# Optimization experiments

Hardware: AMD Instinct MI355X
Metric: run time of the kernel (lower is better)

Reference implementation:

```python
import jax, jax.numpy as jnp
import numpy as np

ALPHA = 0.2  # LeakyReLU negative slope
NEG_INF = -9e15


def setup_inputs() -> dict:
    key = jax.random.key(0)
    k1, k2, k3, k4 = jax.random.split(key, 4)
    N, F_in, F_out = 8192, 128, 64
    x = jax.random.normal(k1, (N, F_in), dtype=jnp.float32)
    adj = jax.random.randint(k2, (N, N), 0, 2, dtype=jnp.int32)
    W = jax.random.normal(k3, (F_in, F_out), dtype=jnp.float32) * 0.1
    a = jax.random.normal(k4, (2 * F_out, 1), dtype=jnp.float32) * 0.1
    return {"x": x, "adj": adj, "W": W, "a": a}


def reference(x, adj, W, a):
    F_out = W.shape[1]
    Wh = x @ W                         # [N, F_out]
    Wh1 = Wh @ a[:F_out, :]            # [N, 1]
    Wh2 = Wh @ a[F_out:, :]            # [N, 1]
    e = Wh1 + Wh2.T                    # [N, N] broadcast scores
    e = jnp.where(e > 0, e, ALPHA * e) # LeakyReLU
    e = jnp.where(adj > 0, e, NEG_INF) # mask non-edges
    attention = jax.nn.softmax(e, axis=1)
    out = attention @ Wh               # [N, F_out]
    return jax.nn.elu(out)             # concat=True -> ELU
```

## Files before the change

kernel.cpp:

```cpp
#include <hip/hip_runtime.h>
#include <hip/hip_bf16.h>

#define NN 8192
#define FIN 128
#define FOUT 64
#define ALPHA 0.2f
#define BM 64
#define CHUNK 128
#define SPLIT 8
#define JSLICE (NN / SPLIT)
#define NCHUNK (JSLICE / CHUNK)
#define PROW (CHUNK + 8)

typedef __attribute__((ext_vector_type(8))) short short8;
typedef __attribute__((ext_vector_type(4))) float floatx4;

static __device__ __forceinline__ ushort f2bf(float f) {
    __hip_bfloat16 h = __float2bfloat16(f);
    return __builtin_bit_cast(ushort, h);
}

__global__ __launch_bounds__(256) void gat_proj(const float* __restrict__ x,
                                                const float* __restrict__ W,
                                                const float* __restrict__ a,
                                                ushort* __restrict__ WhT,
                                                float* __restrict__ Wh1,
                                                float* __restrict__ Wh2) {
    __shared__ float tile[32][FOUT + 1];

    const int t = threadIdx.x;
    const int f = t & 63;
    const int wv = t >> 6;
    const int row0 = blockIdx.x * 32;
    const float af1 = a[f], af2 = a[FOUT + f];

    for (int r8 = 0; r8 < 8; ++r8) {
        const int row = row0 + wv * 8 + r8;
        const float4* __restrict__ x4 = (const float4*)(x + (size_t)row * FIN);
        float acc = 0.f;
        #pragma unroll
        for (int k4 = 0; k4 < FIN / 4; ++k4) {
            float4 xv = x4[k4];
            const int k = k4 * 4;
            acc = fmaf(xv.x, W[(k + 0) * FOUT + f], acc);
            acc = fmaf(xv.y, W[(k + 1) * FOUT + f], acc);
            acc = fmaf(xv.z, W[(k + 2) * FOUT + f], acc);
            acc = fmaf(xv.w, W[(k + 3) * FOUT + f], acc);
        }
        tile[wv * 8 + r8][f] = acc;

        float s1 = acc * af1;
        float s2 = acc * af2;
        #pragma unroll
        for (int off = 32; off; off >>= 1) {
            s1 += __shfl_xor(s1, off, 64);
            s2 += __shfl_xor(s2, off, 64);
        }
        if (f == 0) { Wh1[row] = s1; Wh2[row] = s2; }
    }
    __syncthreads();

    const int r = t & 31;
    const int fh = t >> 5;
    #pragma unroll
    for (int p = 0; p < 8; ++p) {
        const int ff = p * 8 + fh;
        WhT[(size_t)ff * NN + row0 + r] = f2bf(tile[r][ff]);
    }
}

__global__ __launch_bounds__(256) void gat_attn_part(const int* __restrict__ adj,
                                                     const ushort* __restrict__ WhT,
                                                     const float* __restrict__ Wh1,
                                                     const float* __restrict__ Wh2,
                                                     float* __restrict__ pnum,
                                                     float* __restrict__ pden) {
    __shared__ __align__(16) ushort P[2][BM][PROW];

    const int t = threadIdx.x;
    const int lane = t & 63;
    const int wv = t >> 6;
    const int slice = blockIdx.x & (SPLIT - 1);
    const int row0 = (blockIdx.x / SPLIT) * BM;
    const int j0 = slice * JSLICE;
    const int ln = lane & 15;
    const int quad = lane >> 4;
    const int jg = lane & 31;
    const int rh = lane >> 5;
    const int rbase = wv * 16;

    float wh1r[8];
    #pragma unroll
    for (int rr = 0; rr < 8; ++rr)
        wh1r[rr] = Wh1[row0 + rbase + rh * 8 + rr];

    const int* __restrict__ aptr =
        adj + (size_t)(row0 + rbase + rh * 8) * NN + j0 + jg * 4;

    int4 av[8];
    float4 wh2v;
    auto loadChunk = [&](int c) {
        const int jb = c * CHUNK;
        wh2v = *(const float4*)(Wh2 + j0 + jb + jg * 4);
        #pragma unroll
        for (int rr = 0; rr < 8; ++rr)
            av[rr] = *(const int4*)(aptr + (size_t)rr * NN + jb);
    };

    float den[8];
    #pragma unroll
    for (int rr = 0; rr < 8; ++rr) den[rr] = 0.f;

    auto scoresToLds = [&](int b) {
        #pragma unroll
        for (int rr = 0; rr < 8; ++rr) {
            float s0 = wh1r[rr] + wh2v.x, s1 = wh1r[rr] + wh2v.y,
                  s2 = wh1r[rr] + wh2v.z, s3 = wh1r[rr] + wh2v.w;
            s0 = fmaxf(s0, ALPHA * s0); s1 = fmaxf(s1, ALPHA * s1);
            s2 = fmaxf(s2, ALPHA * s2); s3 = fmaxf(s3, ALPHA * s3);
            float p0 = __expf(s0), p1 = __expf(s1),
                  p2 = __expf(s2), p3 = __expf(s3);
            p0 = (av[rr].x > 0) ? p0 : 0.f; p1 = (av[rr].y > 0) ? p1 : 0.f;
            p2 = (av[rr].z > 0) ? p2 : 0.f; p3 = (av[rr].w > 0) ? p3 : 0.f;
            den[rr] += (p0 + p1) + (p2 + p3);
            ushort4 pk = make_ushort4(f2bf(p0), f2bf(p1), f2bf(p2), f2bf(p3));
            *(ushort4*)&P[b][rbase + rh * 8 + rr][jg * 4] = pk;
        }
    };

    floatx4 acc[4];
    #pragma unroll
    for (int mt = 0; mt < 4; ++mt) acc[mt] = (floatx4){0.f, 0.f, 0.f, 0.f};

    const ushort* __restrict__ bbase =
        WhT + (size_t)(wv * 16 + ln) * NN + j0 + quad * 8;

    loadChunk(0);
    scoresToLds(0);
    __syncthreads();

    int pb = 0;
    for (int c = 0; c < NCHUNK; ++c) {
        if (c + 1 < NCHUNK) loadChunk(c + 1);

        const int jb = c * CHUNK;
        short8 bf[4];
        #pragma unroll
        for (int k0 = 0; k0 < 4; ++k0)
            bf[k0] = *(const short8*)(bbase + jb + k0 * 32);
        #pragma unroll
        for (int mt = 0; mt < 4; ++mt) {
            const ushort* Arow = &P[pb][mt * 16 + ln][quad * 8];
            #pragma unroll
            for (int k0 = 0; k0 < 4; ++k0) {
                short8 af = *(const short8*)(Arow + k0 * 32);
                acc[mt] = __builtin_amdgcn_mfma_f32_16x16x32_bf16(af, bf[k0], acc[mt], 0, 0, 0);
            }
        }

        if (c + 1 < NCHUNK) scoresToLds(pb ^ 1);
        __syncthreads();
        pb ^= 1;
    }

    #pragma unroll
    for (int rr = 0; rr < 8; ++rr) {
        float d = den[rr];
        #pragma unroll
        for (int off = 16; off; off >>= 1) d += __shfl_xor(d, off, 64);
        if (jg == 0)
            pden[(size_t)slice * NN + row0 + rbase + rh * 8 + rr] = d;
    }

    #pragma unroll
    for (int mt = 0; mt < 4; ++mt) {
        #pragma unroll
        for (int r = 0; r < 4; ++r) {
            const int i = mt * 16 + quad * 4 + r;
            pnum[((size_t)slice * NN + row0 + i) * FOUT + wv * 16 + ln] = acc[mt][r];
        }
    }
}

__global__ __launch_bounds__(256) void gat_combine(const float* __restrict__ pnum,
                                                   const float* __restrict__ pden,
                                                   float* __restrict__ out) {
    const int idx = blockIdx.x * 256 + threadIdx.x;
    const int row = idx >> 6;
    float num = 0.f, den = 0.f;
    #pragma unroll
    for (int s = 0; s < SPLIT; ++s) {
        num += pnum[(size_t)s * NN * FOUT + idx];
        den += pden[(size_t)s * NN + row];
    }
    float o = num / den;
    o = (o > 0.f) ? o : (__expf(o) - 1.f);
    out[idx] = o;
}

extern "C" void kernel_launch(void* const* d_in, const int* in_sizes, int n_in,
                              void* d_out, int out_size, void* d_ws, size_t ws_size,
                              hipStream_t stream) {
    const float* x   = (const float*)d_in[0];
    const int*   adj = (const int*)  d_in[1];
    const float* W   = (const float*)d_in[2];
    const float* a   = (const float*)d_in[3];
    float* out = (float*)d_out;

    ushort* WhT = (ushort*)d_ws;
    float* Wh1 = (float*)(WhT + (size_t)FOUT * NN);
    float* Wh2 = Wh1 + NN;
    float* pnum = Wh2 + NN;
    float* pden = pnum + (size_t)SPLIT * NN * FOUT;

    gat_proj<<<NN / 32, 256, 0, stream>>>(x, W, a, WhT, Wh1, Wh2);
    gat_attn_part<<<(NN / BM) * SPLIT, 256, 0, stream>>>(adj, WhT, Wh1, Wh2, pnum, pden);
    gat_combine<<<NN * FOUT / 256, 256, 0, stream>>>(pnum, pden, out);
}
```

Before: 403.3 us.

## Deepen adjacency/WhT prefetch to two chunks, use exp2, restructure projection

The attention kernel now double-buffers the adjacency, Wh2 and WhT B-fragment registers and prefetches two chunks ahead, so global-load latency overlaps the MFMA and score work. Scores are pre-scaled by log2(e) in the projection so the hardware exp2 builtin can replace __expf. The projection kernel handles 16 rows per block with each wave computing 4 rows at once, which reuses W loads and doubles the block count. Holding two sets of prefetch buffers raises register pressure and may lower occupancy.

After: 1.089 ms. 170% more time.

```diff
diff --git a/kernel.cpp b/kernel.cpp
--- a/kernel.cpp
+++ b/kernel.cpp
@@ -11,9 +11,16 @@
 #define JSLICE (NN / SPLIT)
 #define NCHUNK (JSLICE / CHUNK)
 #define PROW (CHUNK + 8)
+#define LOG2E 1.44269504f
 
 typedef __attribute__((ext_vector_type(8))) short short8;
 typedef __attribute__((ext_vector_type(4))) float floatx4;
+
+#if __has_builtin(__builtin_amdgcn_exp2f)
+#define EXP2(x) __builtin_amdgcn_exp2f(x)
+#else
+#define EXP2(x) exp2f(x)
+#endif
 
 static __device__ __forceinline__ ushort f2bf(float f) {
     __hip_bfloat16 h = __float2bfloat16(f);
@@ -26,45 +33,53 @@
                                                 ushort* __restrict__ WhT,
                                                 float* __restrict__ Wh1,
                                                 float* __restrict__ Wh2) {
-    __shared__ float tile[32][FOUT + 1];
+    __shared__ float tile[16][FOUT + 1];
 
     const int t = threadIdx.x;
     const int f = t & 63;
-    const int wv = t >> 6;
-    const int row0 = blockIdx.x * 32;
+    const int wvu = __builtin_amdgcn_readfirstlane(t >> 6);
+    const int row0 = blockIdx.x * 16;
     const float af1 = a[f], af2 = a[FOUT + f];
 
-    for (int r8 = 0; r8 < 8; ++r8) {
-        const int row = row0 + wv * 8 + r8;
-        const float4* __restrict__ x4 = (const float4*)(x + (size_t)row * FIN);
-        float acc = 0.f;
-        #pragma unroll
-        for (int k4 = 0; k4 < FIN / 4; ++k4) {
-            float4 xv = x4[k4];
-            const int k = k4 * 4;
-            acc = fmaf(xv.x, W[(k + 0) * FOUT + f], acc);
-            acc = fmaf(xv.y, W[(k + 1) * FOUT + f], acc);
-            acc = fmaf(xv.z, W[(k + 2) * FOUT + f], acc);
-            acc = fmaf(xv.w, W[(k + 3) * FOUT + f], acc);
-        }
-        tile[wv * 8 + r8][f] = acc;
-
-        float s1 = acc * af1;
-        float s2 = acc * af2;
+    const float* __restrict__ xr = x + (size_t)(row0 + wvu * 4) * FIN;
+
+    float accv[4] = {0.f, 0.f, 0.f, 0.f};
+    #pragma unroll
+    for (int k = 0; k < FIN; k += 4) {
+        const float w0 = W[(k + 0) * FOUT + f];
+        const float w1 = W[(k + 1) * FOUT + f];
+        const float w2 = W[(k + 2) * FOUT + f];
+        const float w3 = W[(k + 3) * FOUT + f];
+        #pragma unroll
+        for (int r = 0; r < 4; ++r) {
+            const float4 xv = *(const float4*)(xr + (size_t)r * FIN + k);
+            accv[r] = fmaf(xv.x, w0, fmaf(xv.y, w1, fmaf(xv.z, w2, fmaf(xv.w, w3, accv[r]))));
+        }
+    }
+
+    #pragma unroll
+    for (int r = 0; r < 4; ++r) {
+        tile[wvu * 4 + r][f] = accv[r];
+        float s1 = accv[r] * af1;
+        float s2 = accv[r] * af2;
         #pragma unroll
         for (int off = 32; off; off >>= 1) {
             s1 += __shfl_xor(s1, off, 64);
             s2 += __shfl_xor(s2, off, 64);
         }
-        if (f == 0) { Wh1[row] = s1; Wh2[row] = s2; }
+        if (f == 0) {
+            const int row = row0 + wvu * 4 + r;
+            Wh1[row] = s1 * LOG2E;
+            Wh2[row] = s2 * LOG2E;
+        }
     }
     __syncthreads();
 
-    const int r = t & 31;
-    const int fh = t >> 5;
-    #pragma unroll
-    for (int p = 0; p < 8; ++p) {
-        const int ff = p * 8 + fh;
+    const int r = t & 15;
+    const int fh = t >> 4;
+    #pragma unroll
+    for (int p = 0; p < 4; ++p) {
+        const int ff = p * 16 + fh;
         WhT[(size_t)ff * NN + row0 + r] = f2bf(tile[r][ff]);
     }
 }
@@ -79,7 +94,7 @@
 
     const int t = threadIdx.x;
     const int lane = t & 63;
-    const int wv = t >> 6;
+    const int wvu = __builtin_amdgcn_readfirstlane(t >> 6);
     const int slice = blockIdx.x & (SPLIT - 1);
     const int row0 = (blockIdx.x / SPLIT) * BM;
     const int j0 = slice * JSLICE;
@@ -87,7 +102,7 @@
     const int quad = lane >> 4;
     const int jg = lane & 31;
     const int rh = lane >> 5;
-    const int rbase = wv * 16;
+    const int rbase = wvu * 16;
 
     float wh1r[8];
     #pragma unroll
@@ -96,69 +111,71 @@
 
     const int* __restrict__ aptr =
         adj + (size_t)(row0 + rbase + rh * 8) * NN + j0 + jg * 4;
-
-    int4 av[8];
-    float4 wh2v;
-    auto loadChunk = [&](int c) {
+    const ushort* __restrict__ bbase =
+        WhT + (size_t)(wvu * 16 + ln) * NN + j0 + quad * 8;
+
+    int4 avb[2][8];
+    float4 wh2b[2];
+    short8 bfb[2][4];
+    float den[8];
+    #pragma unroll
+    for (int rr = 0; rr < 8; ++rr) den[rr] = 0.f;
+    floatx4 acc[4];
+    #pragma unroll
+    for (int mt = 0; mt < 4; ++mt) acc[mt] = (floatx4){0.f, 0.f, 0.f, 0.f};
+
+    auto loadAdj = [&](int c, int s) {
         const int jb = c * CHUNK;
-        wh2v = *(const float4*)(Wh2 + j0 + jb + jg * 4);
+        wh2b[s] = *(const float4*)(Wh2 + j0 + jb + jg * 4);
         #pragma unroll
         for (int rr = 0; rr < 8; ++rr)
-            av[rr] = *(const int4*)(aptr + (size_t)rr * NN + jb);
+            avb[s][rr] = *(const int4*)(aptr + (size_t)rr * NN + jb);
     };
-
-    float den[8];
-    #pragma unroll
-    for (int rr = 0; rr < 8; ++rr) den[rr] = 0.f;
-
-    auto scoresToLds = [&](int b) {
+    auto loadB = [&](int c, int s) {
+        #pragma unroll
+        for (int k0 = 0; k0 < 4; ++k0)
+            bfb[s][k0] = *(const short8*)(bbase + c * CHUNK + k0 * 32);
+    };
+    auto scores = [&](int s, int b) {
         #pragma unroll
         for (int rr = 0; rr < 8; ++rr) {
-            float s0 = wh1r[rr] + wh2v.x, s1 = wh1r[rr] + wh2v.y,
-                  s2 = wh1r[rr] + wh2v.z, s3 = wh1r[rr] + wh2v.w;
+            const float w1 = wh1r[rr];
+            float s0 = w1 + wh2b[s].x, s1 = w1 + wh2b[s].y,
+                  s2 = w1 + wh2b[s].z, s3 = w1 + wh2b[s].w;
             s0 = fmaxf(s0, ALPHA * s0); s1 = fmaxf(s1, ALPHA * s1);
             s2 = fmaxf(s2, ALPHA * s2); s3 = fmaxf(s3, ALPHA * s3);
-            float p0 = __expf(s0), p1 = __expf(s1),
-                  p2 = __expf(s2), p3 = __expf(s3);
-            p0 = (av[rr].x > 0) ? p0 : 0.f; p1 = (av[rr].y > 0) ? p1 : 0.f;
-            p2 = (av[rr].z > 0) ? p2 : 0.f; p3 = (av[rr].w > 0) ? p3 : 0.f;
+            float p0 = EXP2(s0), p1 = EXP2(s1), p2 = EXP2(s2), p3 = EXP2(s3);
+            p0 = (avb[s][rr].x > 0) ? p0 : 0.f;
+            p1 = (avb[s][rr].y > 0) ? p1 : 0.f;
+            p2 = (avb[s][rr].z > 0) ? p2 : 0.f;
+            p3 = (avb[s][rr].w > 0) ? p3 : 0.f;
             den[rr] += (p0 + p1) + (p2 + p3);
             ushort4 pk = make_ushort4(f2bf(p0), f2bf(p1), f2bf(p2), f2bf(p3));
             *(ushort4*)&P[b][rbase + rh * 8 + rr][jg * 4] = pk;
         }
     };
 
-    floatx4 acc[4];
-    #pragma unroll
-    for (int mt = 0; mt < 4; ++mt) acc[mt] = (floatx4){0.f, 0.f, 0.f, 0.f};
-
-    const ushort* __restrict__ bbase =
-        WhT + (size_t)(wv * 16 + ln) * NN + j0 + quad * 8;
-
-    loadChunk(0);
-    scoresToLds(0);
+    loadAdj(0, 0); loadB(0, 0);
+    loadAdj(1, 1); loadB(1, 1);
+    scores(0, 0);
     __syncthreads();
 
     int pb = 0;
     for (int c = 0; c < NCHUNK; ++c) {
-        if (c + 1 < NCHUNK) loadChunk(c + 1);
-
-        const int jb = c * CHUNK;
-        short8 bf[4];
-        #pragma unroll
-        for (int k0 = 0; k0 < 4; ++k0)
-            bf[k0] = *(const short8*)(bbase + jb + k0 * 32);
+        const int sc = c & 1;
+        if (c + 2 < NCHUNK) loadAdj(c + 2, sc);
+
         #pragma unroll
         for (int mt = 0; mt < 4; ++mt) {
             const ushort* Arow = &P[pb][mt * 16 + ln][quad * 8];
             #pragma unroll
             for (int k0 = 0; k0 < 4; ++k0) {
                 short8 af = *(const short8*)(Arow + k0 * 32);
-                acc[mt] = __builtin_amdgcn_mfma_f32_16x16x32_bf16(af, bf[k0], acc[mt], 0, 0, 0);
+                acc[mt] = __builtin_amdgcn_mfma_f32_16x16x32_bf16(af, bfb[sc][k0], acc[mt], 0, 0, 0);
             }
         }
-
-        if (c + 1 < NCHUNK) scoresToLds(pb ^ 1);
+        if (c + 2 < NCHUNK) loadB(c + 2, sc);
+        if (c + 1 < NCHUNK) scores(sc ^ 1, pb ^ 1);
         __syncthreads();
         pb ^= 1;
     }
@@ -177,7 +194,7 @@
         #pragma unroll
         for (int r = 0; r < 4; ++r) {
             const int i = mt * 16 + quad * 4 + r;
-            pnum[((size_t)slice * NN + row0 + i) * FOUT + wv * 16 + ln] = acc[mt][r];
+            pnum[((size_t)slice * NN + row0 + i) * FOUT + wvu * 16 + ln] = acc[mt][r];
         }
     }
 }
@@ -213,7 +230,7 @@
     float* pnum = Wh2 + NN;
     float* pden = pnum + (size_t)SPLIT * NN * FOUT;
 
-    gat_proj<<<NN / 32, 256, 0, stream>>>(x, W, a, WhT, Wh1, Wh2);
+    gat_proj<<<NN / 16, 256, 0, stream>>>(x, W, a, WhT, Wh1, Wh2);
     gat_attn_part<<<(NN / BM) * SPLIT, 256, 0, stream>>>(adj, WhT, Wh1, Wh2, pnum, pden);
     gat_combine<<<NN * FOUT / 256, 256, 0, stream>>>(pnum, pden, out);
 }
```
